# Optimization experiments

Measured on AMD Instinct MI355X. Metric: run time of the kernel, lower is better.

## Reference

```python
import jax, jax.numpy as jnp
import numpy as np

B, S, D, H = 4, 2048, 1024, 16
HD = D // H  # head_dim = 64


def setup_inputs() -> dict:
    key = jax.random.key(0)
    ks = jax.random.split(key, 11)
    s = 1.0 / np.sqrt(D)
    return {
        "Q": jax.random.normal(ks[0], (B, S, D), dtype=jnp.float32),
        "K": jax.random.normal(ks[1], (B, S, D), dtype=jnp.float32),
        "V": jax.random.normal(ks[2], (B, S, D), dtype=jnp.float32),
        "Wq": jax.random.normal(ks[3], (D, D), dtype=jnp.float32) * s,
        "bq": jnp.zeros((D,), dtype=jnp.float32),
        "Wk": jax.random.normal(ks[4], (D, D), dtype=jnp.float32) * s,
        "bk": jnp.zeros((D,), dtype=jnp.float32),
        "Wv": jax.random.normal(ks[5], (D, D), dtype=jnp.float32) * s,
        "bv": jnp.zeros((D,), dtype=jnp.float32),
        "Wo": jax.random.normal(ks[6], (D, D), dtype=jnp.float32) * s,
        "bo": jnp.zeros((D,), dtype=jnp.float32),
    }


def _split_heads(x):
    # [B, S, D] -> [B, H, S, HD]
    b, s, _ = x.shape
    return x.reshape(b, s, H, HD).transpose(0, 2, 1, 3)


def reference(Q, K, V, Wq, bq, Wk, bk, Wv, bv, Wo, bo):
    q = _split_heads(Q @ Wq + bq)  # [B,H,S,HD]
    k = _split_heads(K @ Wk + bk)
    v = _split_heads(V @ Wv + bv)
    scale = 1.0 / jnp.sqrt(jnp.float32(HD))
    scores = jnp.einsum('bhqd,bhkd->bhqk', q, k) * scale  # [B,H,S,S]
    attn = jax.nn.softmax(scores, axis=-1)
    out = jnp.einsum('bhqk,bhkd->bhqd', attn, v)  # [B,H,S,HD]
    out = out.transpose(0, 2, 1, 3).reshape(Q.shape[0], -1, D)  # [B,S,D]
    return out @ Wo + bo
```

## Files before the change

### kernel.cpp

```cpp
#include <hip/hip_runtime.h>
#include <hip/hip_bf16.h>

typedef unsigned short u16;
typedef unsigned int u32;
typedef u16 u16x4 __attribute__((ext_vector_type(4)));
typedef u16 u16x8 __attribute__((ext_vector_type(8)));
typedef u32 u32x4 __attribute__((ext_vector_type(4)));
typedef float f32x4 __attribute__((ext_vector_type(4)));
typedef float f32x16 __attribute__((ext_vector_type(16)));
typedef __bf16 bf16x8 __attribute__((ext_vector_type(8)));

#define MFMA16(A, B, C) __builtin_amdgcn_mfma_f32_16x16x32_bf16( \
    __builtin_bit_cast(bf16x8, (A)), __builtin_bit_cast(bf16x8, (B)), (C), 0, 0, 0)
#define MFMA32(A, B, C) __builtin_amdgcn_mfma_f32_32x32x16_bf16( \
    __builtin_bit_cast(bf16x8, (A)), __builtin_bit_cast(bf16x8, (B)), (C), 0, 0, 0)

__device__ __forceinline__ u16 f2bf(float f) {
    u32 u = __float_as_uint(f);
    u += 0x7fffu + ((u >> 16) & 1u);
    return (u16)(u >> 16);
}

__device__ __forceinline__ u32 cvtpk(float lo, float hi) {
    u32 d;
    asm("v_cvt_pk_bf16_f32 %0, %1, %2" : "=v"(d) : "v"(lo), "v"(hi));
    return d;
}

__device__ __forceinline__ void gll16(const void* g, void* l) {
    __builtin_amdgcn_global_load_lds(
        (const __attribute__((address_space(1))) void*)g,
        (__attribute__((address_space(3))) void*)l, 16, 0, 0);
}

__global__ void f2bf3(const float* __restrict__ a0, const float* __restrict__ a1,
                      const float* __restrict__ a2, u16* __restrict__ o0,
                      u16* __restrict__ o1, u16* __restrict__ o2, int n4) {
    const float* in = (blockIdx.y == 0) ? a0 : (blockIdx.y == 1) ? a1 : a2;
    u16* out = (blockIdx.y == 0) ? o0 : (blockIdx.y == 1) ? o1 : o2;
    int i = blockIdx.x * blockDim.x + threadIdx.x;
    int stride = gridDim.x * blockDim.x;
    for (; i < n4; i += stride) {
        float4 v = ((const float4*)in)[i];
        u16x4 o;
        o[0] = f2bf(v.x); o[1] = f2bf(v.y); o[2] = f2bf(v.z); o[3] = f2bf(v.w);
        ((u16x4*)out)[i] = o;
    }
}

__global__ void cvt_wt(const float* __restrict__ W0, const float* __restrict__ W1,
                       const float* __restrict__ W2, const float* __restrict__ W3,
                       u16* __restrict__ T0, u16* __restrict__ T1,
                       u16* __restrict__ T2, u16* __restrict__ T3) {
    const int z = blockIdx.z;
    const float* W = (z == 0) ? W0 : (z == 1) ? W1 : (z == 2) ? W2 : W3;
    u16* T = (z == 0) ? T0 : (z == 1) ? T1 : (z == 2) ? T2 : T3;
    __shared__ float tile[64][65];
    const int n0 = blockIdx.x * 64, k0 = blockIdx.y * 64;
    const int tx = threadIdx.x & 63, ty = threadIdx.x >> 6;
#pragma unroll
    for (int i = 0; i < 16; ++i) {
        int r = i * 4 + ty;
        tile[r][tx] = W[(size_t)(k0 + r) * 1024 + n0 + tx];
    }
    __syncthreads();
#pragma unroll
    for (int i = 0; i < 16; ++i) {
        int r = i * 4 + ty;
        T[(size_t)(n0 + r) * 1024 + k0 + tx] = f2bf(tile[tx][r]);
    }
}

__device__ __forceinline__ void gemm_core(
    const u16* __restrict__ A, const u16* __restrict__ Bt,
    const float* __restrict__ bias, void* __restrict__ out,
    int mode, float scale, int bm, int bn, u16* lAs, u16* lBs) {
    const int tid = threadIdx.x, lane = tid & 63, wid = tid >> 6;
    const int wr = wid >> 1, wc = wid & 1;
    const int l15 = lane & 15, l16 = lane >> 4;

    f32x4 acc[4][4];
#pragma unroll
    for (int i = 0; i < 4; ++i)
#pragma unroll
        for (int j = 0; j < 4; ++j) acc[i][j] = f32x4{0.f, 0.f, 0.f, 0.f};

    const char* Ab = (const char*)A;
    const char* Bb = (const char*)Bt;
    char* ldsA = (char*)lAs;
    char* ldsB = (char*)lBs;
    const int rA0 = wid * 32 + (lane >> 3);
    const int ci = ((lane & 7) ^ (lane >> 3)) * 16;

    for (int k0 = 0; k0 < 1024; k0 += 64) {
        __syncthreads();
#pragma unroll
        for (int c = 0; c < 4; ++c) {
            int row = rA0 + c * 8;
            gll16(Ab + ((size_t)(bm + row) * 1024 + k0) * 2 + ci, ldsA + (wid * 4 + c) * 1024);
            gll16(Bb + ((size_t)(bn + row) * 1024 + k0) * 2 + ci, ldsB + (wid * 4 + c) * 1024);
        }
        asm volatile("s_waitcnt vmcnt(0)" ::: "memory");
        __syncthreads();

#pragma unroll
        for (int kk = 0; kk < 2; ++kk) {
            u16x8 af[4], bf[4];
#pragma unroll
            for (int mi = 0; mi < 4; ++mi) {
                int row = wr * 64 + mi * 16 + l15;
                int cg = kk * 4 + l16;
                af[mi] = *(const u16x8*)(ldsA + row * 128 + ((cg ^ (row & 7)) * 16));
            }
#pragma unroll
            for (int ni = 0; ni < 4; ++ni) {
                int row = wc * 64 + ni * 16 + l15;
                int cg = kk * 4 + l16;
                bf[ni] = *(const u16x8*)(ldsB + row * 128 + ((cg ^ (row & 7)) * 16));
            }
#pragma unroll
            for (int mi = 0; mi < 4; ++mi)
#pragma unroll
                for (int ni = 0; ni < 4; ++ni)
                    acc[mi][ni] = MFMA16(af[mi], bf[ni], acc[mi][ni]);
        }
    }

    const int row0 = bm + wr * 64, col0 = bn + wc * 64;
#pragma unroll
    for (int ni = 0; ni < 4; ++ni) {
        int col = col0 + ni * 16 + l15;
        float bv = bias[col];
#pragma unroll
        for (int mi = 0; mi < 4; ++mi) {
            int rowb = row0 + mi * 16 + l16 * 4;
            if (mode == 1) {
                int b = rowb >> 11, s = rowb & 2047, h = col >> 6, d = col & 63;
                u16x4 pv;
#pragma unroll
                for (int r = 0; r < 4; ++r) pv[r] = f2bf((acc[mi][ni][r] + bv) * scale);
                *(u16x4*)((u16*)out + (((size_t)(b * 16 + h)) * 64 + d) * 2048 + s) = pv;
            } else {
#pragma unroll
                for (int r = 0; r < 4; ++r) {
                    int row = rowb + r;
                    float v = (acc[mi][ni][r] + bv) * scale;
                    if (mode == 2) {
                        ((float*)out)[(size_t)row * 1024 + col] = v;
                    } else {
                        int b = row >> 11, s = row & 2047, h = col >> 6, d = col & 63;
                        ((u16*)out)[(((size_t)(b * 16 + h)) * 2048 + s) * 64 + d] = f2bf(v);
                    }
                }
            }
        }
    }
}

__device__ __forceinline__ void xcd_decode(int wg, int& bm, int& bn) {
    int xcd = wg & 7, pos = wg >> 3;
    bm = (xcd * 8 + (pos >> 3)) * 128;
    bn = (pos & 7) * 128;
}

__global__ __launch_bounds__(256, 3) void gemm_qkv(
    const u16* __restrict__ XQ, const u16* __restrict__ XK, const u16* __restrict__ XV,
    const u16* __restrict__ WQ, const u16* __restrict__ WK, const u16* __restrict__ WV,
    const float* __restrict__ bq, const float* __restrict__ bk, const float* __restrict__ bv,
    u16* __restrict__ qo, u16* __restrict__ ko, u16* __restrict__ vo, float qscale) {
    __shared__ u16 lAs[128 * 64];
    __shared__ u16 lBs[128 * 64];
    const int z = blockIdx.z;
    const u16* A = (z == 0) ? XQ : (z == 1) ? XK : XV;
    const u16* Bt = (z == 0) ? WQ : (z == 1) ? WK : WV;
    const float* bias = (z == 0) ? bq : (z == 1) ? bk : bv;
    u16* out = (z == 0) ? qo : (z == 1) ? ko : vo;
    const int mode = (z == 2) ? 1 : 0;
    const float scale = (z == 0) ? qscale : 1.0f;
    int bm, bn;
    xcd_decode(blockIdx.y * 8 + blockIdx.x, bm, bn);
    gemm_core(A, Bt, bias, out, mode, scale, bm, bn, lAs, lBs);
}

__global__ __launch_bounds__(256, 3) void gemm_out(
    const u16* __restrict__ A, const u16* __restrict__ Bt,
    const float* __restrict__ bias, float* __restrict__ out) {
    __shared__ u16 lAs[128 * 64];
    __shared__ u16 lBs[128 * 64];
    int bm, bn;
    xcd_decode(blockIdx.y * 8 + blockIdx.x, bm, bn);
    gemm_core(A, Bt, bias, out, 2, 1.0f, bm, bn, lAs, lBs);
}

__global__ __launch_bounds__(256, 4) void attn_fwd(
    const u16* __restrict__ qh, const u16* __restrict__ kh,
    const u16* __restrict__ vth, u16* __restrict__ ao) {
    __shared__ u16 lK[2][64 * 64];
    __shared__ u16 lV[2][64 * 64];
    const int tid = threadIdx.x, lane = tid & 63, wid = tid >> 6;
    const int l31 = lane & 31, l32 = lane >> 5;
    const int wg = blockIdx.x;
    const int xcd = wg & 7, pos = wg >> 3;
    const int bh = xcd * 8 + (pos >> 4);
    const int xblk = pos & 15;
    const int q0 = xblk * 128 + wid * 32;
    const char* kb = (const char*)(kh + (size_t)bh * 2048 * 64);
    const char* vb = (const char*)(vth + (size_t)bh * 64 * 2048);
    const u16* qb = qh + (size_t)bh * 2048 * 64;

    u16x8 qf[4];
#pragma unroll
    for (int kc = 0; kc < 4; ++kc)
        qf[kc] = *(const u16x8*)(qb + (size_t)(q0 + l31) * 64 + kc * 16 + l32 * 8);

    float l_run = 0.f;
    f32x16 oacc[2] = {};

    char* ldsK = (char*)lK;
    char* ldsV = (char*)lV;
    const int srow = wid * 16 + (lane >> 3);
    const int sci = ((lane & 7) ^ (lane >> 3)) * 16;

#define STAGE(kv0, bo) do { \
    _Pragma("unroll") \
    for (int c = 0; c < 2; ++c) { \
        int row = srow + c * 8; \
        gll16(kb + (size_t)((kv0) + row) * 128 + sci, ldsK + (bo) + (wid * 2 + c) * 1024); \
        gll16(vb + (size_t)row * 4096 + (size_t)(kv0) * 2 + sci, ldsV + (bo) + (wid * 2 + c) * 1024); \
    } } while (0)

    STAGE(0, 0);
    int cur = 0;

    for (int it = 0; it < 32; ++it) {
        if (it < 31) {
            STAGE((it + 1) * 64, (cur ^ 1) * 8192);
            asm volatile("s_waitcnt vmcnt(4)" ::: "memory");
        } else {
            asm volatile("s_waitcnt vmcnt(0)" ::: "memory");
        }
        __syncthreads();
        const char* K_ = ldsK + cur * 8192;
        const char* V_ = ldsV + cur * 8192;

        f32x16 s[2] = {};
        __builtin_amdgcn_s_setprio(1);
#pragma unroll
        for (int kc = 0; kc < 4; ++kc) {
#pragma unroll
            for (int sub = 0; sub < 2; ++sub) {
                int row = sub * 32 + l31;
                int cg = kc * 2 + l32;
                u16x8 kf = *(const u16x8*)(K_ + row * 128 + ((cg ^ (row & 7)) * 16));
                s[sub] = MFMA32(kf, qf[kc], s[sub]);
            }
        }
        __builtin_amdgcn_s_setprio(0);

        float p0[16], p1[16];
#pragma unroll
        for (int r = 0; r < 16; ++r) p0[r] = __builtin_amdgcn_exp2f(s[0][r]);
#pragma unroll
        for (int r = 0; r < 16; ++r) p1[r] = __builtin_amdgcn_exp2f(s[1][r]);

        u16x8 pa[2][2];
#pragma unroll
        for (int c2 = 0; c2 < 2; ++c2) {
            u32 x0 = cvtpk(p0[c2 * 8 + 0], p0[c2 * 8 + 1]);
            u32 x1 = cvtpk(p0[c2 * 8 + 2], p0[c2 * 8 + 3]);
            u32 y0 = cvtpk(p0[c2 * 8 + 4], p0[c2 * 8 + 5]);
            u32 y1 = cvtpk(p0[c2 * 8 + 6], p0[c2 * 8 + 7]);
            asm("v_permlane32_swap_b32 %0, %1" : "+v"(x0), "+v"(y0));
            asm("v_permlane32_swap_b32 %0, %1" : "+v"(x1), "+v"(y1));
            u32x4 wa = {x0, x1, y0, y1};
            pa[0][c2] = __builtin_bit_cast(u16x8, wa);
            u32 z0 = cvtpk(p1[c2 * 8 + 0], p1[c2 * 8 + 1]);
            u32 z1 = cvtpk(p1[c2 * 8 + 2], p1[c2 * 8 + 3]);
            u32 v0 = cvtpk(p1[c2 * 8 + 4], p1[c2 * 8 + 5]);
            u32 v1 = cvtpk(p1[c2 * 8 + 6], p1[c2 * 8 + 7]);
            asm("v_permlane32_swap_b32 %0, %1" : "+v"(z0), "+v"(v0));
            asm("v_permlane32_swap_b32 %0, %1" : "+v"(z1), "+v"(v1));
            u32x4 wb = {z0, z1, v0, v1};
            pa[1][c2] = __builtin_bit_cast(u16x8, wb);
        }

        float a8[8];
#pragma unroll
        for (int i = 0; i < 8; ++i)
            a8[i] = (p0[i] + p0[i + 8]) + (p1[i] + p1[i + 8]);
        float ls = ((a8[0] + a8[4]) + (a8[1] + a8[5])) +
                   ((a8[2] + a8[6]) + (a8[3] + a8[7]));
        ls += __shfl_xor(ls, 32);
        l_run += ls;

        __builtin_amdgcn_s_setprio(1);
#pragma unroll
        for (int dsub = 0; dsub < 2; ++dsub) {
#pragma unroll
            for (int sub = 0; sub < 2; ++sub) {
#pragma unroll
                for (int c2 = 0; c2 < 2; ++c2) {
                    int row = dsub * 32 + l31;
                    int cg = sub * 4 + c2 * 2 + l32;
                    u16x8 vf = *(const u16x8*)(V_ + row * 128 + ((cg ^ (row & 7)) * 16));
                    oacc[dsub] = MFMA32(pa[sub][c2], vf, oacc[dsub]);
                }
            }
        }
        __builtin_amdgcn_s_setprio(0);
        __syncthreads();
        cur ^= 1;
    }
#undef STAGE

    const int b = bh >> 4, h = bh & 15;
    float inv = 1.f / l_run;
#pragma unroll
    for (int r = 0; r < 16; ++r) {
        int rq = ((r & 3) + 8 * (r >> 2)) + 4 * l32;
        float fr = __shfl(inv, rq);
        int sq = q0 + rq;
#pragma unroll
        for (int dsub = 0; dsub < 2; ++dsub) {
            int d = dsub * 32 + l31;
            ao[((size_t)(b * 2048 + sq)) * 1024 + h * 64 + d] = f2bf(oacc[dsub][r] * fr);
        }
    }
}

extern "C" void kernel_launch(void* const* d_in, const int* in_sizes, int n_in,
                              void* d_out, int out_size, void* d_ws, size_t ws_size,
                              hipStream_t stream) {
    const float* Q  = (const float*)d_in[0];
    const float* K  = (const float*)d_in[1];
    const float* V  = (const float*)d_in[2];
    const float* Wq = (const float*)d_in[3];
    const float* bq = (const float*)d_in[4];
    const float* Wk = (const float*)d_in[5];
    const float* bk = (const float*)d_in[6];
    const float* Wv = (const float*)d_in[7];
    const float* bv = (const float*)d_in[8];
    const float* Wo = (const float*)d_in[9];
    const float* bo = (const float*)d_in[10];

    char* ws = (char*)d_ws;
    const size_t MB = 1024u * 1024u;
    u16* XQ  = (u16*)(ws);
    u16* XK  = (u16*)(ws + 16 * MB);
    u16* XV  = (u16*)(ws + 32 * MB);
    u16* WTQ = (u16*)(ws + 48 * MB);
    u16* WTK = (u16*)(ws + 50 * MB);
    u16* WTV = (u16*)(ws + 52 * MB);
    u16* WTO = (u16*)(ws + 54 * MB);
    u16* qhp = (u16*)(ws + 56 * MB);
    u16* khp = (u16*)(ws + 72 * MB);
    u16* vtp = (u16*)(ws + 88 * MB);
    u16* aop = XQ;

    const float qscale = 0.125f * 1.44269504088896f;

    cvt_wt<<<dim3(16, 16, 4), 256, 0, stream>>>(Wq, Wk, Wv, Wo, WTQ, WTK, WTV, WTO);
    f2bf3<<<dim3(2048, 3), 256, 0, stream>>>(Q, K, V, XQ, XK, XV, 2097152);

    gemm_qkv<<<dim3(8, 64, 3), 256, 0, stream>>>(XQ, XK, XV, WTQ, WTK, WTV,
                                                 bq, bk, bv, qhp, khp, vtp, qscale);

    attn_fwd<<<1024, 256, 0, stream>>>(qhp, khp, vtp, aop);

    gemm_out<<<dim3(8, 64), 256, 0, stream>>>(aop, WTO, bo, (float*)d_out);
}
```

Measured before the change: 183.8 us.

## Triple-buffer attention K/V tiles to drop trailing barrier; merge prep kernels

The attention kernel moves from double to triple buffering of K/V tiles in LDS, which lets it drop the end-of-iteration __syncthreads. It also initialises the score accumulator by passing zero into the first MFMA. The input-conversion and weight-transpose kernels are merged into one launch to save launch overhead. The larger LDS footprint lowers the occupancy bound from 4 to 3 blocks, and the prep grid launches many idle blocks.

```diff
diff --git a/kernel.cpp b/kernel.cpp
--- a/kernel.cpp
+++ b/kernel.cpp
@@ -33,30 +33,34 @@
         (__attribute__((address_space(3))) void*)l, 16, 0, 0);
 }
 
-__global__ void f2bf3(const float* __restrict__ a0, const float* __restrict__ a1,
-                      const float* __restrict__ a2, u16* __restrict__ o0,
-                      u16* __restrict__ o1, u16* __restrict__ o2, int n4) {
-    const float* in = (blockIdx.y == 0) ? a0 : (blockIdx.y == 1) ? a1 : a2;
-    u16* out = (blockIdx.y == 0) ? o0 : (blockIdx.y == 1) ? o1 : o2;
-    int i = blockIdx.x * blockDim.x + threadIdx.x;
-    int stride = gridDim.x * blockDim.x;
-    for (; i < n4; i += stride) {
-        float4 v = ((const float4*)in)[i];
-        u16x4 o;
-        o[0] = f2bf(v.x); o[1] = f2bf(v.y); o[2] = f2bf(v.z); o[3] = f2bf(v.w);
-        ((u16x4*)out)[i] = o;
-    }
-}
-
-__global__ void cvt_wt(const float* __restrict__ W0, const float* __restrict__ W1,
-                       const float* __restrict__ W2, const float* __restrict__ W3,
-                       u16* __restrict__ T0, u16* __restrict__ T1,
-                       u16* __restrict__ T2, u16* __restrict__ T3) {
-    const int z = blockIdx.z;
+__global__ void prep(const float* __restrict__ Q, const float* __restrict__ K,
+                     const float* __restrict__ V, u16* __restrict__ XQ,
+                     u16* __restrict__ XK, u16* __restrict__ XV,
+                     const float* __restrict__ W0, const float* __restrict__ W1,
+                     const float* __restrict__ W2, const float* __restrict__ W3,
+                     u16* __restrict__ T0, u16* __restrict__ T1,
+                     u16* __restrict__ T2, u16* __restrict__ T3) {
+    if (blockIdx.y < 3) {
+        const float* in = (blockIdx.y == 0) ? Q : (blockIdx.y == 1) ? K : V;
+        u16* out = (blockIdx.y == 0) ? XQ : (blockIdx.y == 1) ? XK : XV;
+        const int n4 = 2097152;
+        int i = blockIdx.x * blockDim.x + threadIdx.x;
+        int stride = gridDim.x * blockDim.x;
+        for (; i < n4; i += stride) {
+            float4 v = ((const float4*)in)[i];
+            u16x4 o;
+            o[0] = f2bf(v.x); o[1] = f2bf(v.y); o[2] = f2bf(v.z); o[3] = f2bf(v.w);
+            ((u16x4*)out)[i] = o;
+        }
+        return;
+    }
+    const int wg = blockIdx.x;
+    if (wg >= 1024) return;
+    const int z = wg >> 8;
     const float* W = (z == 0) ? W0 : (z == 1) ? W1 : (z == 2) ? W2 : W3;
     u16* T = (z == 0) ? T0 : (z == 1) ? T1 : (z == 2) ? T2 : T3;
     __shared__ float tile[64][65];
-    const int n0 = blockIdx.x * 64, k0 = blockIdx.y * 64;
+    const int n0 = ((wg >> 4) & 15) * 64, k0 = (wg & 15) * 64;
     const int tx = threadIdx.x & 63, ty = threadIdx.x >> 6;
 #pragma unroll
     for (int i = 0; i < 16; ++i) {
@@ -192,11 +196,11 @@
     gemm_core(A, Bt, bias, out, 2, 1.0f, bm, bn, lAs, lBs);
 }
 
-__global__ __launch_bounds__(256, 4) void attn_fwd(
+__global__ __launch_bounds__(256, 3) void attn_fwd(
     const u16* __restrict__ qh, const u16* __restrict__ kh,
     const u16* __restrict__ vth, u16* __restrict__ ao) {
-    __shared__ u16 lK[2][64 * 64];
-    __shared__ u16 lV[2][64 * 64];
+    __shared__ u16 lK[3][64 * 64];
+    __shared__ u16 lV[3][64 * 64];
     const int tid = threadIdx.x, lane = tid & 63, wid = tid >> 6;
     const int l31 = lane & 31, l32 = lane >> 5;
     const int wg = blockIdx.x;
@@ -214,7 +218,11 @@
         qf[kc] = *(const u16x8*)(qb + (size_t)(q0 + l31) * 64 + kc * 16 + l32 * 8);
 
     float l_run = 0.f;
-    f32x16 oacc[2] = {};
+    f32x16 zero16;
+#pragma unroll
+    for (int r = 0; r < 16; ++r) zero16[r] = 0.f;
+    f32x16 oacc[2];
+    oacc[0] = zero16; oacc[1] = zero16;
 
     char* ldsK = (char*)lK;
     char* ldsV = (char*)lV;
@@ -230,20 +238,22 @@
     } } while (0)
 
     STAGE(0, 0);
-    int cur = 0;
+    int cslot = 0, nslot = 1;
 
     for (int it = 0; it < 32; ++it) {
         if (it < 31) {
-            STAGE((it + 1) * 64, (cur ^ 1) * 8192);
+            STAGE((it + 1) * 64, nslot * 8192);
             asm volatile("s_waitcnt vmcnt(4)" ::: "memory");
         } else {
             asm volatile("s_waitcnt vmcnt(0)" ::: "memory");
         }
         __syncthreads();
-        const char* K_ = ldsK + cur * 8192;
-        const char* V_ = ldsV + cur * 8192;
-
-        f32x16 s[2] = {};
+        const char* K_ = ldsK + cslot * 8192;
+        const char* V_ = ldsV + cslot * 8192;
+        cslot = nslot;
+        nslot = (nslot == 2) ? 0 : nslot + 1;
+
+        f32x16 s[2];
         __builtin_amdgcn_s_setprio(1);
 #pragma unroll
         for (int kc = 0; kc < 4; ++kc) {
@@ -252,7 +262,7 @@
                 int row = sub * 32 + l31;
                 int cg = kc * 2 + l32;
                 u16x8 kf = *(const u16x8*)(K_ + row * 128 + ((cg ^ (row & 7)) * 16));
-                s[sub] = MFMA32(kf, qf[kc], s[sub]);
+                s[sub] = MFMA32(kf, qf[kc], (kc == 0) ? zero16 : s[sub]);
             }
         }
         __builtin_amdgcn_s_setprio(0);
@@ -308,8 +318,6 @@
             }
         }
         __builtin_amdgcn_s_setprio(0);
-        __syncthreads();
-        cur ^= 1;
     }
 #undef STAGE
 
@@ -359,8 +367,8 @@
 
     const float qscale = 0.125f * 1.44269504088896f;
 
-    cvt_wt<<<dim3(16, 16, 4), 256, 0, stream>>>(Wq, Wk, Wv, Wo, WTQ, WTK, WTV, WTO);
-    f2bf3<<<dim3(2048, 3), 256, 0, stream>>>(Q, K, V, XQ, XK, XV, 2097152);
+    prep<<<dim3(2048, 4), 256, 0, stream>>>(Q, K, V, XQ, XK, XV,
+                                            Wq, Wk, Wv, Wo, WTQ, WTK, WTV, WTO);
 
     gemm_qkv<<<dim3(8, 64, 3), 256, 0, stream>>>(XQ, XK, XV, WTQ, WTK, WTV,
                                                  bq, bk, bv, qhp, khp, vtp, qscale);
```

Measured after the change: 190.6 us. 1.04x slower.
